# Kernel optimization log

Hardware: AMD Instinct MI355X
Metric: run time of the kernel (lower is better)

Reference implementation:

```python
import jax, jax.numpy as jnp
import numpy as np

B, N, D, CF = 8, 2048, 512, 128  # batch, nodes, feat_dim, count_feat


def setup_inputs() -> dict:
    key = jax.random.key(0)
    ks = jax.random.split(key, 12)
    s = 1.0 / np.sqrt(D)
    return {
        "X": jax.random.normal(ks[0], (B, N, D), jnp.float32),
        # first MultiHeadAttention (num_heads=1, mode='QK', out_features=feat_dim)
        "Wq1": jax.random.normal(ks[1], (D, D), jnp.float32) * s,
        "Wk1": jax.random.normal(ks[2], (D, D), jnp.float32) * s,
        "Wv1": jax.random.normal(ks[3], (D, D), jnp.float32) * s,
        "Wo1": jax.random.normal(ks[4], (D, D), jnp.float32) * s,
        # score attention (only its raw QK^T scores are used downstream)
        "Wq2": jax.random.normal(ks[5], (D, D), jnp.float32) * s,
        "Wk2": jax.random.normal(ks[6], (D, D), jnp.float32) * s,
        # count_mlp: Linear(D,CF) -> LeakyReLU(0.1) -> Linear(CF,1)
        "W1": jax.random.normal(ks[7], (D, CF), jnp.float32) * s,
        "b1": jnp.zeros((CF,), jnp.float32),
        "W2": jax.random.normal(ks[8], (CF, 1), jnp.float32) * (1.0 / np.sqrt(CF)),
        "b2": jnp.zeros((1,), jnp.float32),
    }


def reference(X, Wq1, Wk1, Wv1, Wo1, Wq2, Wk2, W1, b1, W2, b2):
    scale = 1.0 / jnp.sqrt(jnp.asarray(X.shape[-1], X.dtype))
    # --- first self-attention: att = softmax(QK^T/sqrt(d)) V Wo ---
    q1 = X @ Wq1
    k1 = X @ Wk1
    v1 = X @ Wv1
    s1 = jnp.einsum("bnd,bmd->bnm", q1, k1) * scale      # [B,N,N]
    p1 = jax.nn.softmax(s1, axis=-1)
    att = jnp.einsum("bnm,bmd->bnd", p1, v1) @ Wo1        # [B,N,D]
    # --- score attention over att: only raw scores are consumed ---
    s2 = jnp.einsum("bnd,bmd->bnm", att @ Wq2, att @ Wk2) * scale  # [B,N,N]
    # --- count_mlp threshold per node ---
    h = att @ W1 + b1
    h = jnp.where(h >= 0, h, 0.1 * h)                     # LeakyReLU(0.1)
    thresh = h @ W2 + b2                                  # [B,N,1]
    # --- mlp_score_thresh readout: clamp, row-normalize, clip ---
    surv = jnp.maximum(s2 - thresh, 0.0)                  # broadcast over last dim
    A = jnp.clip(surv / (jnp.sum(surv, axis=-1, keepdims=True) + 1e-9), 0.0, 1.0)
    return A
```

## Files before the change

kernel.cpp:

```cpp
#include <hip/hip_runtime.h>
#include <hip/hip_bf16.h>

#define BB 8
#define NN 2048
#define DD 512
#define CFF 128
#define MT (BB*NN)

typedef _Float16 half_t;
typedef __attribute__((ext_vector_type(8))) _Float16 half8;
typedef __attribute__((ext_vector_type(4))) float floatx4;
typedef __attribute__((ext_vector_type(4))) unsigned int uint4v;

#define MFMA16(a,b,c) __builtin_amdgcn_mfma_f32_16x16x32_f16((a),(b),(c),0,0,0)

template<int EPI>
__global__ __launch_bounds__(256) void gemm_f16s(
    const half_t* __restrict__ Ahi, const half_t* __restrict__ Alo, long lda, long sA,
    const half_t* __restrict__ Bhi, const half_t* __restrict__ Blo, long ldb, long sB,
    float* __restrict__ Cf, half_t* __restrict__ Chi, half_t* __restrict__ Clo, long ldc, long sC,
    int K, float alpha, const float* __restrict__ bias, const float* __restrict__ tvec)
{
    const int tid = threadIdx.x;
    const int row0 = blockIdx.y * 128, col0 = blockIdx.x * 128;
    const long z = blockIdx.z;
    const half_t* pAh = Ahi + z * sA + (long)row0 * lda;
    const half_t* pAl = Alo + z * sA + (long)row0 * lda;
    const half_t* pBh = Bhi + z * sB + (long)col0 * ldb;
    const half_t* pBl = Blo + z * sB + (long)col0 * ldb;

    __shared__ half_t lds[2][4][4096];

    const int l  = tid & 63;
    const int w  = tid >> 6;
    const int wr = w >> 1, wc = w & 1;
    const int Rw = wr * 64, Cw = wc * 64;
    const int rl = l & 15, kc = l >> 4;
    const int swz = (kc ^ (rl & 3)) * 8;

    floatx4 acc[4][4];
#pragma unroll
    for (int m = 0; m < 4; ++m)
#pragma unroll
        for (int n = 0; n < 4; ++n) acc[m][n] = (floatx4){0.f, 0.f, 0.f, 0.f};

    const int r0s = tid >> 2,         c0s = tid & 3;
    const int r1s = (tid + 256) >> 2, c1s = tid & 3;
    const int off0 = r0s * 32 + ((c0s ^ (r0s & 3)) * 8);
    const int off1 = r1s * 32 + ((c1s ^ (r1s & 3)) * 8);

    auto stage = [&](int buf, int k0) {
        long ga0 = (long)r0s * lda + k0 + c0s * 8;
        long gb0 = (long)r0s * ldb + k0 + c0s * 8;
        long ga1 = (long)r1s * lda + k0 + c1s * 8;
        long gb1 = (long)r1s * ldb + k0 + c1s * 8;
        uint4v a0 = *(const uint4v*)(pAh + ga0);
        uint4v a1 = *(const uint4v*)(pAl + ga0);
        uint4v b0 = *(const uint4v*)(pBh + gb0);
        uint4v b1 = *(const uint4v*)(pBl + gb0);
        uint4v a2 = *(const uint4v*)(pAh + ga1);
        uint4v a3 = *(const uint4v*)(pAl + ga1);
        uint4v b2 = *(const uint4v*)(pBh + gb1);
        uint4v b3 = *(const uint4v*)(pBl + gb1);
        *(uint4v*)&lds[buf][0][off0] = a0;
        *(uint4v*)&lds[buf][1][off0] = a1;
        *(uint4v*)&lds[buf][2][off0] = b0;
        *(uint4v*)&lds[buf][3][off0] = b1;
        *(uint4v*)&lds[buf][0][off1] = a2;
        *(uint4v*)&lds[buf][1][off1] = a3;
        *(uint4v*)&lds[buf][2][off1] = b2;
        *(uint4v*)&lds[buf][3][off1] = b3;
    };

    const int nk = K >> 5;
    stage(0, 0);
#pragma unroll 2
    for (int t = 0; t < nk; ++t) {
        __syncthreads();
        const int cur = t & 1;
        const half_t* bAh = &lds[cur][0][0];
        const half_t* bAl = &lds[cur][1][0];
        const half_t* bBh = &lds[cur][2][0];
        const half_t* bBl = &lds[cur][3][0];
        half8 af[4][2], bf[4][2];
#pragma unroll
        for (int m = 0; m < 4; ++m) {
            int off = (Rw + m * 16 + rl) * 32 + swz;
            af[m][0] = *(const half8*)(bAh + off);
            af[m][1] = *(const half8*)(bAl + off);
        }
#pragma unroll
        for (int n = 0; n < 4; ++n) {
            int off = (Cw + n * 16 + rl) * 32 + swz;
            bf[n][0] = *(const half8*)(bBh + off);
            bf[n][1] = *(const half8*)(bBl + off);
        }
#pragma unroll
        for (int m = 0; m < 4; ++m)
#pragma unroll
            for (int n = 0; n < 4; ++n) {
                acc[m][n] = MFMA16(af[m][0], bf[n][0], acc[m][n]);
                acc[m][n] = MFMA16(af[m][1], bf[n][0], acc[m][n]);
                acc[m][n] = MFMA16(af[m][0], bf[n][1], acc[m][n]);
            }
        if (t + 1 < nk) stage((t + 1) & 1, (t + 1) << 5);
    }

    const float* tv = (EPI == 3) ? (tvec + z * NN) : tvec;
#pragma unroll
    for (int m = 0; m < 4; ++m) {
#pragma unroll
        for (int n = 0; n < 4; ++n) {
            int col = col0 + Cw + n * 16 + rl;
#pragma unroll
            for (int r = 0; r < 4; ++r) {
                int row = row0 + Rw + m * 16 + kc * 4 + r;
                float v = acc[m][n][r];
                if (EPI == 0) {
                    Cf[z * sC + (long)row * ldc + col] = v * alpha;
                } else if (EPI == 1) {
                    half_t hh = (half_t)v;
                    long o = z * sC + (long)row * ldc + col;
                    Chi[o] = hh;
                    Clo[o] = (half_t)(v - (float)hh);
                } else if (EPI == 2) {
                    v += bias[col];
                    Cf[(long)row * ldc + col] = (v >= 0.f) ? v : 0.1f * v;
                } else {
                    Cf[z * sC + (long)row * ldc + col] = fmaxf(v * alpha - tv[row], 0.f);
                }
            }
        }
    }
}

__device__ __forceinline__ float waveReduceMax(float v) {
#pragma unroll
    for (int o = 32; o; o >>= 1) v = fmaxf(v, __shfl_down(v, o));
    return v;
}
__device__ __forceinline__ float waveReduceSum(float v) {
#pragma unroll
    for (int o = 32; o; o >>= 1) v += __shfl_down(v, o);
    return v;
}

__global__ __launch_bounds__(256) void softmax_split_kernel(float* __restrict__ S)
{
    __shared__ float red[4];
    __shared__ float fin;
    long row = blockIdx.x;
    float* p = S + row * (long)NN;
    half_t* ph = (half_t*)p;
    half_t* pl = ph + NN;
    int t = threadIdx.x;

    float4 v0 = *reinterpret_cast<float4*>(p + t * 8);
    float4 v1 = *reinterpret_cast<float4*>(p + t * 8 + 4);

    float m = fmaxf(fmaxf(fmaxf(v0.x, v0.y), fmaxf(v0.z, v0.w)),
                    fmaxf(fmaxf(v1.x, v1.y), fmaxf(v1.z, v1.w)));
    m = waveReduceMax(m);
    if ((t & 63) == 0) red[t >> 6] = m;
    __syncthreads();
    if (t == 0) fin = fmaxf(fmaxf(red[0], red[1]), fmaxf(red[2], red[3]));
    __syncthreads();
    m = fin;

    float e[8];
    e[0] = __expf(v0.x - m); e[1] = __expf(v0.y - m); e[2] = __expf(v0.z - m); e[3] = __expf(v0.w - m);
    e[4] = __expf(v1.x - m); e[5] = __expf(v1.y - m); e[6] = __expf(v1.z - m); e[7] = __expf(v1.w - m);
    float s = ((e[0] + e[1]) + (e[2] + e[3])) + ((e[4] + e[5]) + (e[6] + e[7]));
    s = waveReduceSum(s);
    __syncthreads();
    if ((t & 63) == 0) red[t >> 6] = s;
    __syncthreads();
    if (t == 0) fin = (red[0] + red[1]) + (red[2] + red[3]);
    __syncthreads();
    float inv = 1.0f / fin;

    __syncthreads();
    half8 hv, lv;
#pragma unroll
    for (int j = 0; j < 8; ++j) {
        float pv = e[j] * inv;
        half_t hh = (half_t)pv;
        hv[j] = hh;
        lv[j] = (half_t)(pv - (float)hh);
    }
    *(half8*)(ph + t * 8) = hv;
    *(half8*)(pl + t * 8) = lv;
}

__global__ __launch_bounds__(256) void rowsum_kernel(const float* __restrict__ S, float* __restrict__ sums)
{
    __shared__ float red[4];
    long row = blockIdx.x;
    const float* p = S + row * (long)NN;
    int t = threadIdx.x;
    float4 v0 = *reinterpret_cast<const float4*>(p + t * 8);
    float4 v1 = *reinterpret_cast<const float4*>(p + t * 8 + 4);
    float s = ((v0.x + v0.y) + (v0.z + v0.w)) + ((v1.x + v1.y) + (v1.z + v1.w));
    s = waveReduceSum(s);
    if ((t & 63) == 0) red[t >> 6] = s;
    __syncthreads();
    if (t == 0) sums[row] = (red[0] + red[1]) + (red[2] + red[3]);
}

__global__ __launch_bounds__(256) void norm_kernel(float* __restrict__ S, const float* __restrict__ sums)
{
    long i = (long)blockIdx.x * 256 + threadIdx.x;
    long base = i * 4;
    long row = base >> 11;
    float inv = 1.0f / (sums[row] + 1e-9f);
    float4 v = *reinterpret_cast<float4*>(S + base);
    v.x = fminf(v.x * inv, 1.0f);
    v.y = fminf(v.y * inv, 1.0f);
    v.z = fminf(v.z * inv, 1.0f);
    v.w = fminf(v.w * inv, 1.0f);
    *reinterpret_cast<float4*>(S + base) = v;
}

__global__ __launch_bounds__(64) void thresh_kernel(const float* __restrict__ h,
                                                    const float* __restrict__ W2,
                                                    const float* __restrict__ b2,
                                                    float* __restrict__ th)
{
    int row = blockIdx.x;
    int t = threadIdx.x;
    const float* hp = h + (long)row * CFF;
    float v = hp[t] * W2[t] + hp[t + 64] * W2[t + 64];
    v = waveReduceSum(v);
    if (t == 0) th[row] = v + b2[0];
}

__global__ __launch_bounds__(256) void wprep(const float* __restrict__ W,
                                             half_t* __restrict__ Th, half_t* __restrict__ Tl,
                                             int K, int N)
{
    __shared__ float tw[32][33];
    int n0 = blockIdx.x * 32, k0 = blockIdx.y * 32;
    int c = threadIdx.x & 31, r8 = threadIdx.x >> 5;
#pragma unroll
    for (int i = 0; i < 4; ++i) {
        int r = r8 + i * 8;
        tw[r][c] = W[(long)(k0 + r) * N + n0 + c];
    }
    __syncthreads();
#pragma unroll
    for (int i = 0; i < 4; ++i) {
        int nr = r8 + i * 8;
        float v = tw[c][nr];
        half_t hh = (half_t)v;
        Th[(long)(n0 + nr) * K + k0 + c] = hh;
        Tl[(long)(n0 + nr) * K + k0 + c] = (half_t)(v - (float)hh);
    }
}

__global__ __launch_bounds__(256) void split_f32(const float* __restrict__ in,
                                                 half_t* __restrict__ hi, half_t* __restrict__ lo)
{
    long i = ((long)blockIdx.x * 256 + threadIdx.x) * 8;
    float4 a = *(const float4*)(in + i), b = *(const float4*)(in + i + 4);
    float v[8] = {a.x, a.y, a.z, a.w, b.x, b.y, b.z, b.w};
    half8 hv, lv;
#pragma unroll
    for (int j = 0; j < 8; ++j) {
        half_t hh = (half_t)v[j];
        hv[j] = hh;
        lv[j] = (half_t)(v[j] - (float)hh);
    }
    *(half8*)(hi + i) = hv;
    *(half8*)(lo + i) = lv;
}

__global__ __launch_bounds__(256) void transpose_pair(const half_t* __restrict__ ih, const half_t* __restrict__ il,
                                                      half_t* __restrict__ oh, half_t* __restrict__ ol)
{
    __shared__ half_t th[64][66], tl[64][66];
    int b = blockIdx.z;
    int c0 = blockIdx.x * 64;
    int r0 = blockIdx.y * 64;
    const half_t* pih = ih + ((long)b * 2048 + r0) * 512 + c0;
    const half_t* pil = il + ((long)b * 2048 + r0) * 512 + c0;
    int t = threadIdx.x;
    int cc = (t & 7) * 8, rr = t >> 3;
#pragma unroll
    for (int i = 0; i < 2; ++i) {
        int r = rr + 32 * i;
        *(uint4v*)&th[r][cc] = *(const uint4v*)(pih + (long)r * 512 + cc);
        *(uint4v*)&tl[r][cc] = *(const uint4v*)(pil + (long)r * 512 + cc);
    }
    __syncthreads();
    half_t* poh = oh + ((long)b * 512 + c0) * 2048 + r0;
    half_t* pol = ol + ((long)b * 512 + c0) * 2048 + r0;
#pragma unroll
    for (int i = 0; i < 2; ++i) {
        int ic = rr + 32 * i;
        half8 vh, vl;
#pragma unroll
        for (int j = 0; j < 8; ++j) {
            vh[j] = th[cc + j][ic];
            vl[j] = tl[cc + j][ic];
        }
        *(half8*)(poh + (long)ic * 2048 + cc) = vh;
        *(half8*)(pol + (long)ic * 2048 + cc) = vl;
    }
}

static void launch_gemm16(hipStream_t s, int epi,
    const half_t* Ahi, const half_t* Alo, long lda, long sA,
    const half_t* Bhi, const half_t* Blo, long ldb, long sB,
    float* Cf, half_t* Chi, half_t* Clo, long ldc, long sC,
    int M, int N, int K, int batch, float alpha, const float* bias, const float* tvec)
{
    dim3 g(N / 128, M / 128, batch), b(256, 1, 1);
    if (epi == 0)      gemm_f16s<0><<<g, b, 0, s>>>(Ahi, Alo, lda, sA, Bhi, Blo, ldb, sB, Cf, Chi, Clo, ldc, sC, K, alpha, bias, tvec);
    else if (epi == 1) gemm_f16s<1><<<g, b, 0, s>>>(Ahi, Alo, lda, sA, Bhi, Blo, ldb, sB, Cf, Chi, Clo, ldc, sC, K, alpha, bias, tvec);
    else if (epi == 2) gemm_f16s<2><<<g, b, 0, s>>>(Ahi, Alo, lda, sA, Bhi, Blo, ldb, sB, Cf, Chi, Clo, ldc, sC, K, alpha, bias, tvec);
    else               gemm_f16s<3><<<g, b, 0, s>>>(Ahi, Alo, lda, sA, Bhi, Blo, ldb, sB, Cf, Chi, Clo, ldc, sC, K, alpha, bias, tvec);
}

extern "C" void kernel_launch(void* const* d_in, const int* in_sizes, int n_in,
                              void* d_out, int out_size, void* d_ws, size_t ws_size,
                              hipStream_t stream)
{
    const float* X   = (const float*)d_in[0];
    const float* Wq1 = (const float*)d_in[1];
    const float* Wk1 = (const float*)d_in[2];
    const float* Wv1 = (const float*)d_in[3];
    const float* Wo1 = (const float*)d_in[4];
    const float* Wq2 = (const float*)d_in[5];
    const float* Wk2 = (const float*)d_in[6];
    const float* W1  = (const float*)d_in[7];
    const float* b1  = (const float*)d_in[8];
    const float* W2  = (const float*)d_in[9];
    const float* b2  = (const float*)d_in[10];

    float* out = (float*)d_out;
    const float scale = 0.044194173824159216f;

    half_t* wsH = (half_t*)d_ws;
    const long U  = (long)MT * DD;
    const long WD = (long)DD * DD;
    half_t* sAh = wsH;          half_t* sAl = wsH + U;
    half_t* sBh = wsH + 2 * U;  half_t* sBl = wsH + 3 * U;
    half_t* sCh = wsH + 4 * U;  half_t* sCl = wsH + 5 * U;
    half_t* wt  = wsH + 6 * U;
    half_t* wq1h = wt;              half_t* wq1l = wq1h + WD;
    half_t* wk1h = wq1l + WD;       half_t* wk1l = wk1h + WD;
    half_t* wv1h = wk1l + WD;       half_t* wv1l = wv1h + WD;
    half_t* wo1h = wv1l + WD;       half_t* wo1l = wo1h + WD;
    half_t* wq2h = wo1l + WD;       half_t* wq2l = wq2h + WD;
    half_t* wk2h = wq2l + WD;       half_t* wk2l = wk2h + WD;
    half_t* w1h  = wk2l + WD;       half_t* w1l  = w1h + (long)DD * CFF;
    float*  thresh = (float*)(w1l + (long)DD * CFF);
    float*  sums   = thresh + MT;
    float* h = out;

    split_f32<<<dim3(4096), dim3(256), 0, stream>>>(X, sAh, sAl);
    wprep<<<dim3(16, 16), dim3(256), 0, stream>>>(Wq1, wq1h, wq1l, DD, DD);
    wprep<<<dim3(16, 16), dim3(256), 0, stream>>>(Wk1, wk1h, wk1l, DD, DD);
    wprep<<<dim3(16, 16), dim3(256), 0, stream>>>(Wv1, wv1h, wv1l, DD, DD);
    wprep<<<dim3(16, 16), dim3(256), 0, stream>>>(Wo1, wo1h, wo1l, DD, DD);
    wprep<<<dim3(16, 16), dim3(256), 0, stream>>>(Wq2, wq2h, wq2l, DD, DD);
    wprep<<<dim3(16, 16), dim3(256), 0, stream>>>(Wk2, wk2h, wk2l, DD, DD);
    wprep<<<dim3(4, 16),  dim3(256), 0, stream>>>(W1,  w1h,  w1l,  DD, CFF);

    launch_gemm16(stream, 1, sAh, sAl, DD, 0, wq1h, wq1l, DD, 0,
                  nullptr, sBh, sBl, DD, 0, MT, DD, DD, 1, 1.f, nullptr, nullptr);
    launch_gemm16(stream, 1, sAh, sAl, DD, 0, wk1h, wk1l, DD, 0,
                  nullptr, sCh, sCl, DD, 0, MT, DD, DD, 1, 1.f, nullptr, nullptr);

    launch_gemm16(stream, 0, sBh, sBl, DD, (long)NN * DD, sCh, sCl, DD, (long)NN * DD,
                  out, nullptr, nullptr, NN, (long)NN * NN, NN, NN, DD, BB, scale, nullptr, nullptr);

    launch_gemm16(stream, 1, sAh, sAl, DD, 0, wv1h, wv1l, DD, 0,
                  nullptr, sBh, sBl, DD, 0, MT, DD, DD, 1, 1.f, nullptr, nullptr);

    softmax_split_kernel<<<dim3(MT), dim3(256), 0, stream>>>(out);

    transpose_pair<<<dim3(8, 32, BB), dim3(256), 0, stream>>>(sBh, sBl, sCh, sCl);

    {
        const half_t* p1h = (const half_t*)d_out;
        const half_t* p1l = p1h + NN;
        launch_gemm16(stream, 1, p1h, p1l, 2 * NN, (long)NN * 2 * NN,
                      sCh, sCl, NN, (long)DD * NN,
                      nullptr, sBh, sBl, DD, (long)NN * DD, NN, DD, NN, BB, 1.f, nullptr, nullptr);
    }

    launch_gemm16(stream, 1, sBh, sBl, DD, 0, wo1h, wo1l, DD, 0,
                  nullptr, sCh, sCl, DD, 0, MT, DD, DD, 1, 1.f, nullptr, nullptr);

    launch_gemm16(stream, 1, sCh, sCl, DD, 0, wq2h, wq2l, DD, 0,
                  nullptr, sAh, sAl, DD, 0, MT, DD, DD, 1, 1.f, nullptr, nullptr);
    launch_gemm16(stream, 1, sCh, sCl, DD, 0, wk2h, wk2l, DD, 0,
                  nullptr, sBh, sBl, DD, 0, MT, DD, DD, 1, 1.f, nullptr, nullptr);

    launch_gemm16(stream, 2, sCh, sCl, DD, 0, w1h, w1l, DD, 0,
                  h, nullptr, nullptr, CFF, 0, MT, CFF, DD, 1, 1.f, b1, nullptr);

    thresh_kernel<<<dim3(MT), dim3(64), 0, stream>>>(h, W2, b2, thresh);

    launch_gemm16(stream, 3, sAh, sAl, DD, (long)NN * DD, sBh, sBl, DD, (long)NN * DD,
                  out, nullptr, nullptr, NN, (long)NN * NN, NN, NN, DD, BB, scale, nullptr, thresh);

    rowsum_kernel<<<dim3(MT), dim3(256), 0, stream>>>(out, sums);
    norm_kernel<<<dim3(out_size / 1024), dim3(256), 0, stream>>>(out, sums);
}
```

Before: 900.0 us.

## Fuse QK projections, thresh MLP and rowsum into GEMM epilogues; swizzle block order

Merges the Q/K projection GEMMs of both attentions into single wider GEMMs whose outputs are routed to separate slots, and folds the count-MLP second layer plus bias into the W1 GEMM epilogue through shuffle-reduced atomicAdds. The score GEMM epilogue now accumulates per-row sums with atomics, which removes the separate rowsum pass over the 128MB score matrix. It also adds a block-index remap across the grid and widens the norm kernel to 8 elements per thread. The atomics make the summation order nondeterministic and need a zero/bias initialisation kernel.

```diff
diff --git a/kernel.cpp b/kernel.cpp
--- a/kernel.cpp
+++ b/kernel.cpp
@@ -18,12 +18,23 @@
 __global__ __launch_bounds__(256) void gemm_f16s(
     const half_t* __restrict__ Ahi, const half_t* __restrict__ Alo, long lda, long sA,
     const half_t* __restrict__ Bhi, const half_t* __restrict__ Blo, long ldb, long sB,
-    float* __restrict__ Cf, half_t* __restrict__ Chi, half_t* __restrict__ Clo, long ldc, long sC,
-    int K, float alpha, const float* __restrict__ bias, const float* __restrict__ tvec)
-{
+    float* __restrict__ Cf, half_t* __restrict__ Chi, half_t* __restrict__ Clo,
+    long ldc, long sC, long slotS,
+    int K, float alpha, const float* __restrict__ bias, const float* __restrict__ tvec,
+    float* __restrict__ rsum)
+{
+    const int gx = gridDim.x, gy = gridDim.y;
+    int d = blockIdx.x + gx * (blockIdx.y + gy * blockIdx.z);
+    int total = gx * gy * gridDim.z;
+    int t0 = (d & 7) * (total >> 3) + (d >> 3);
+    int bx = t0 % gx;
+    int t1 = t0 / gx;
+    int by = t1 % gy;
+    int bz = t1 / gy;
+
     const int tid = threadIdx.x;
-    const int row0 = blockIdx.y * 128, col0 = blockIdx.x * 128;
-    const long z = blockIdx.z;
+    const int row0 = by * 128, col0 = bx * 128;
+    const long z = bz;
     const half_t* pAh = Ahi + z * sA + (long)row0 * lda;
     const half_t* pAl = Alo + z * sA + (long)row0 * lda;
     const half_t* pBh = Bhi + z * sB + (long)col0 * ldb;
@@ -106,29 +117,84 @@
         if (t + 1 < nk) stage((t + 1) & 1, (t + 1) << 5);
     }
 
-    const float* tv = (EPI == 3) ? (tvec + z * NN) : tvec;
-#pragma unroll
-    for (int m = 0; m < 4; ++m) {
-#pragma unroll
-        for (int n = 0; n < 4; ++n) {
-            int col = col0 + Cw + n * 16 + rl;
+    if (EPI == 0) {
+#pragma unroll
+        for (int m = 0; m < 4; ++m)
+#pragma unroll
+            for (int n = 0; n < 4; ++n) {
+                int col = col0 + Cw + n * 16 + rl;
+#pragma unroll
+                for (int r = 0; r < 4; ++r) {
+                    int row = row0 + Rw + m * 16 + kc * 4 + r;
+                    Cf[z * sC + (long)row * ldc + col] = acc[m][n][r] * alpha;
+                }
+            }
+    } else if (EPI == 1) {
+#pragma unroll
+        for (int m = 0; m < 4; ++m)
+#pragma unroll
+            for (int n = 0; n < 4; ++n) {
+                int col = col0 + Cw + n * 16 + rl;
+                long obase = (long)(col >> 9) * slotS + z * sC + (col & 511);
+#pragma unroll
+                for (int r = 0; r < 4; ++r) {
+                    int row = row0 + Rw + m * 16 + kc * 4 + r;
+                    long o = obase + (long)row * ldc;
+                    float v = acc[m][n][r];
+                    half_t hh = (half_t)v;
+                    Chi[o] = hh;
+                    Clo[o] = (half_t)(v - (float)hh);
+                }
+            }
+    } else if (EPI == 3) {
+        const float* tv = tvec + z * NN;
+        float* rs = rsum + z * NN;
+#pragma unroll
+        for (int m = 0; m < 4; ++m) {
 #pragma unroll
             for (int r = 0; r < 4; ++r) {
                 int row = row0 + Rw + m * 16 + kc * 4 + r;
-                float v = acc[m][n][r];
-                if (EPI == 0) {
-                    Cf[z * sC + (long)row * ldc + col] = v * alpha;
-                } else if (EPI == 1) {
-                    half_t hh = (half_t)v;
-                    long o = z * sC + (long)row * ldc + col;
-                    Chi[o] = hh;
-                    Clo[o] = (half_t)(v - (float)hh);
-                } else if (EPI == 2) {
-                    v += bias[col];
-                    Cf[(long)row * ldc + col] = (v >= 0.f) ? v : 0.1f * v;
-                } else {
-                    Cf[z * sC + (long)row * ldc + col] = fmaxf(v * alpha - tv[row], 0.f);
+                float tvr = tv[row];
+                float partial = 0.f;
+#pragma unroll
+                for (int n = 0; n < 4; ++n) {
+                    int col = col0 + Cw + n * 16 + rl;
+                    float v = fmaxf(acc[m][n][r] * alpha - tvr, 0.f);
+                    Cf[z * sC + (long)row * ldc + col] = v;
+                    partial += v;
                 }
+                partial += __shfl_xor(partial, 1);
+                partial += __shfl_xor(partial, 2);
+                partial += __shfl_xor(partial, 4);
+                partial += __shfl_xor(partial, 8);
+                if (rl == 0) atomicAdd(&rs[row], partial);
+            }
+        }
+    } else {
+        float w2v[4], bv[4];
+#pragma unroll
+        for (int n = 0; n < 4; ++n) {
+            int col = Cw + n * 16 + rl;
+            bv[n]  = bias[col];
+            w2v[n] = tvec[col];
+        }
+#pragma unroll
+        for (int m = 0; m < 4; ++m) {
+#pragma unroll
+            for (int r = 0; r < 4; ++r) {
+                int row = row0 + Rw + m * 16 + kc * 4 + r;
+                float partial = 0.f;
+#pragma unroll
+                for (int n = 0; n < 4; ++n) {
+                    float v = acc[m][n][r] + bv[n];
+                    v = (v >= 0.f) ? v : 0.1f * v;
+                    partial += v * w2v[n];
+                }
+                partial += __shfl_xor(partial, 1);
+                partial += __shfl_xor(partial, 2);
+                partial += __shfl_xor(partial, 4);
+                partial += __shfl_xor(partial, 8);
+                if (rl == 0) atomicAdd(&rsum[row], partial);
             }
         }
     }
@@ -192,46 +258,27 @@
     *(half8*)(pl + t * 8) = lv;
 }
 
-__global__ __launch_bounds__(256) void rowsum_kernel(const float* __restrict__ S, float* __restrict__ sums)
-{
-    __shared__ float red[4];
-    long row = blockIdx.x;
-    const float* p = S + row * (long)NN;
-    int t = threadIdx.x;
-    float4 v0 = *reinterpret_cast<const float4*>(p + t * 8);
-    float4 v1 = *reinterpret_cast<const float4*>(p + t * 8 + 4);
-    float s = ((v0.x + v0.y) + (v0.z + v0.w)) + ((v1.x + v1.y) + (v1.z + v1.w));
-    s = waveReduceSum(s);
-    if ((t & 63) == 0) red[t >> 6] = s;
-    __syncthreads();
-    if (t == 0) sums[row] = (red[0] + red[1]) + (red[2] + red[3]);
-}
-
 __global__ __launch_bounds__(256) void norm_kernel(float* __restrict__ S, const float* __restrict__ sums)
 {
     long i = (long)blockIdx.x * 256 + threadIdx.x;
-    long base = i * 4;
+    long base = i * 8;
     long row = base >> 11;
     float inv = 1.0f / (sums[row] + 1e-9f);
-    float4 v = *reinterpret_cast<float4*>(S + base);
-    v.x = fminf(v.x * inv, 1.0f);
-    v.y = fminf(v.y * inv, 1.0f);
-    v.z = fminf(v.z * inv, 1.0f);
-    v.w = fminf(v.w * inv, 1.0f);
-    *reinterpret_cast<float4*>(S + base) = v;
-}
-
-__global__ __launch_bounds__(64) void thresh_kernel(const float* __restrict__ h,
-                                                    const float* __restrict__ W2,
-                                                    const float* __restrict__ b2,
-                                                    float* __restrict__ th)
-{
-    int row = blockIdx.x;
-    int t = threadIdx.x;
-    const float* hp = h + (long)row * CFF;
-    float v = hp[t] * W2[t] + hp[t + 64] * W2[t + 64];
-    v = waveReduceSum(v);
-    if (t == 0) th[row] = v + b2[0];
+    float4 v0 = *reinterpret_cast<float4*>(S + base);
+    float4 v1 = *reinterpret_cast<float4*>(S + base + 4);
+    v0.x = fminf(v0.x * inv, 1.0f); v0.y = fminf(v0.y * inv, 1.0f);
+    v0.z = fminf(v0.z * inv, 1.0f); v0.w = fminf(v0.w * inv, 1.0f);
+    v1.x = fminf(v1.x * inv, 1.0f); v1.y = fminf(v1.y * inv, 1.0f);
+    v1.z = fminf(v1.z * inv, 1.0f); v1.w = fminf(v1.w * inv, 1.0f);
+    *reinterpret_cast<float4*>(S + base) = v0;
+    *reinterpret_cast<float4*>(S + base + 4) = v1;
+}
+
+__global__ __launch_bounds__(256) void init_aux(float* __restrict__ thresh, float* __restrict__ sums,
+                                                const float* __restrict__ b2)
+{
+    int i = blockIdx.x * 256 + threadIdx.x;
+    if (i < MT) { thresh[i] = b2[0]; sums[i] = 0.f; }
 }
 
 __global__ __launch_bounds__(256) void wprep(const float* __restrict__ W,
@@ -311,14 +358,15 @@
 static void launch_gemm16(hipStream_t s, int epi,
     const half_t* Ahi, const half_t* Alo, long lda, long sA,
     const half_t* Bhi, const half_t* Blo, long ldb, long sB,
-    float* Cf, half_t* Chi, half_t* Clo, long ldc, long sC,
-    int M, int N, int K, int batch, float alpha, const float* bias, const float* tvec)
+    float* Cf, half_t* Chi, half_t* Clo, long ldc, long sC, long slotS,
+    int M, int N, int K, int batch, float alpha,
+    const float* bias, const float* tvec, float* rsum)
 {
     dim3 g(N / 128, M / 128, batch), b(256, 1, 1);
-    if (epi == 0)      gemm_f16s<0><<<g, b, 0, s>>>(Ahi, Alo, lda, sA, Bhi, Blo, ldb, sB, Cf, Chi, Clo, ldc, sC, K, alpha, bias, tvec);
-    else if (epi == 1) gemm_f16s<1><<<g, b, 0, s>>>(Ahi, Alo, lda, sA, Bhi, Blo, ldb, sB, Cf, Chi, Clo, ldc, sC, K, alpha, bias, tvec);
-    else if (epi == 2) gemm_f16s<2><<<g, b, 0, s>>>(Ahi, Alo, lda, sA, Bhi, Blo, ldb, sB, Cf, Chi, Clo, ldc, sC, K, alpha, bias, tvec);
-    else               gemm_f16s<3><<<g, b, 0, s>>>(Ahi, Alo, lda, sA, Bhi, Blo, ldb, sB, Cf, Chi, Clo, ldc, sC, K, alpha, bias, tvec);
+    if (epi == 0)      gemm_f16s<0><<<g, b, 0, s>>>(Ahi, Alo, lda, sA, Bhi, Blo, ldb, sB, Cf, Chi, Clo, ldc, sC, slotS, K, alpha, bias, tvec, rsum);
+    else if (epi == 1) gemm_f16s<1><<<g, b, 0, s>>>(Ahi, Alo, lda, sA, Bhi, Blo, ldb, sB, Cf, Chi, Clo, ldc, sC, slotS, K, alpha, bias, tvec, rsum);
+    else if (epi == 3) gemm_f16s<3><<<g, b, 0, s>>>(Ahi, Alo, lda, sA, Bhi, Blo, ldb, sB, Cf, Chi, Clo, ldc, sC, slotS, K, alpha, bias, tvec, rsum);
+    else               gemm_f16s<4><<<g, b, 0, s>>>(Ahi, Alo, lda, sA, Bhi, Blo, ldb, sB, Cf, Chi, Clo, ldc, sC, slotS, K, alpha, bias, tvec, rsum);
 }
 
 extern "C" void kernel_launch(void* const* d_in, const int* in_sizes, int n_in,
@@ -347,36 +395,32 @@
     half_t* sBh = wsH + 2 * U;  half_t* sBl = wsH + 3 * U;
     half_t* sCh = wsH + 4 * U;  half_t* sCl = wsH + 5 * U;
     half_t* wt  = wsH + 6 * U;
-    half_t* wq1h = wt;              half_t* wq1l = wq1h + WD;
-    half_t* wk1h = wq1l + WD;       half_t* wk1l = wk1h + WD;
-    half_t* wv1h = wk1l + WD;       half_t* wv1l = wv1h + WD;
-    half_t* wo1h = wv1l + WD;       half_t* wo1l = wo1h + WD;
-    half_t* wq2h = wo1l + WD;       half_t* wq2l = wq2h + WD;
-    half_t* wk2h = wq2l + WD;       half_t* wk2l = wk2h + WD;
-    half_t* w1h  = wk2l + WD;       half_t* w1l  = w1h + (long)DD * CFF;
+    half_t* wqk1h = wt;               half_t* wqk1l = wqk1h + 2 * WD;
+    half_t* wv1h  = wqk1l + 2 * WD;   half_t* wv1l  = wv1h + WD;
+    half_t* wo1h  = wv1l + WD;        half_t* wo1l  = wo1h + WD;
+    half_t* wqk2h = wo1l + WD;        half_t* wqk2l = wqk2h + 2 * WD;
+    half_t* w1h   = wqk2l + 2 * WD;   half_t* w1l   = w1h + (long)DD * CFF;
     float*  thresh = (float*)(w1l + (long)DD * CFF);
     float*  sums   = thresh + MT;
-    float* h = out;
-
+
+    init_aux<<<dim3(64), dim3(256), 0, stream>>>(thresh, sums, b2);
     split_f32<<<dim3(4096), dim3(256), 0, stream>>>(X, sAh, sAl);
-    wprep<<<dim3(16, 16), dim3(256), 0, stream>>>(Wq1, wq1h, wq1l, DD, DD);
-    wprep<<<dim3(16, 16), dim3(256), 0, stream>>>(Wk1, wk1h, wk1l, DD, DD);
-    wprep<<<dim3(16, 16), dim3(256), 0, stream>>>(Wv1, wv1h, wv1l, DD, DD);
-    wprep<<<dim3(16, 16), dim3(256), 0, stream>>>(Wo1, wo1h, wo1l, DD, DD);
-    wprep<<<dim3(16, 16), dim3(256), 0, stream>>>(Wq2, wq2h, wq2l, DD, DD);
-    wprep<<<dim3(16, 16), dim3(256), 0, stream>>>(Wk2, wk2h, wk2l, DD, DD);
-    wprep<<<dim3(4, 16),  dim3(256), 0, stream>>>(W1,  w1h,  w1l,  DD, CFF);
-
-    launch_gemm16(stream, 1, sAh, sAl, DD, 0, wq1h, wq1l, DD, 0,
-                  nullptr, sBh, sBl, DD, 0, MT, DD, DD, 1, 1.f, nullptr, nullptr);
-    launch_gemm16(stream, 1, sAh, sAl, DD, 0, wk1h, wk1l, DD, 0,
-                  nullptr, sCh, sCl, DD, 0, MT, DD, DD, 1, 1.f, nullptr, nullptr);
+    wprep<<<dim3(16, 16), dim3(256), 0, stream>>>(Wq1, wqk1h,      wqk1l,      DD, DD);
+    wprep<<<dim3(16, 16), dim3(256), 0, stream>>>(Wk1, wqk1h + WD, wqk1l + WD, DD, DD);
+    wprep<<<dim3(16, 16), dim3(256), 0, stream>>>(Wv1, wv1h,  wv1l,  DD, DD);
+    wprep<<<dim3(16, 16), dim3(256), 0, stream>>>(Wo1, wo1h,  wo1l,  DD, DD);
+    wprep<<<dim3(16, 16), dim3(256), 0, stream>>>(Wq2, wqk2h,      wqk2l,      DD, DD);
+    wprep<<<dim3(16, 16), dim3(256), 0, stream>>>(Wk2, wqk2h + WD, wqk2l + WD, DD, DD);
+    wprep<<<dim3(4, 16),  dim3(256), 0, stream>>>(W1,  w1h,   w1l,   DD, CFF);
+
+    launch_gemm16(stream, 1, sAh, sAl, DD, 0, wqk1h, wqk1l, DD, 0,
+                  nullptr, sBh, sBl, DD, 0, 2 * U, MT, 2 * DD, DD, 1, 1.f, nullptr, nullptr, nullptr);
 
     launch_gemm16(stream, 0, sBh, sBl, DD, (long)NN * DD, sCh, sCl, DD, (long)NN * DD,
-                  out, nullptr, nullptr, NN, (long)NN * NN, NN, NN, DD, BB, scale, nullptr, nullptr);
+                  out, nullptr, nullptr, NN, (long)NN * NN, 0, NN, NN, DD, BB, scale, nullptr, nullptr, nullptr);
 
     launch_gemm16(stream, 1, sAh, sAl, DD, 0, wv1h, wv1l, DD, 0,
-                  nullptr, sBh, sBl, DD, 0, MT, DD, DD, 1, 1.f, nullptr, nullptr);
+                  nullptr, sBh, sBl, DD, 0, 0, MT, DD, DD, 1, 1.f, nullptr, nullptr, nullptr);
 
     softmax_split_kernel<<<dim3(MT), dim3(256), 0, stream>>>(out);
 
@@ -387,25 +431,20 @@
         const half_t* p1l = p1h + NN;
         launch_gemm16(stream, 1, p1h, p1l, 2 * NN, (long)NN * 2 * NN,
                       sCh, sCl, NN, (long)DD * NN,
-                      nullptr, sBh, sBl, DD, (long)NN * DD, NN, DD, NN, BB, 1.f, nullptr, nullptr);
+                      nullptr, sBh, sBl, DD, (long)NN * DD, 0, NN, DD, NN, BB, 1.f, nullptr, nullptr, nullptr);
     }
 
     launch_gemm16(stream, 1, sBh, sBl, DD, 0, wo1h, wo1l, DD, 0,
-                  nullptr, sCh, sCl, DD, 0, MT, DD, DD, 1, 1.f, nullptr, nullptr);
-
-    launch_gemm16(stream, 1, sCh, sCl, DD, 0, wq2h, wq2l, DD, 0,
-                  nullptr, sAh, sAl, DD, 0, MT, DD, DD, 1, 1.f, nullptr, nullptr);
-    launch_gemm16(stream, 1, sCh, sCl, DD, 0, wk2h, wk2l, DD, 0,
-                  nullptr, sBh, sBl, DD, 0, MT, DD, DD, 1, 1.f, nullptr, nullptr);
-
-    launch_gemm16(stream, 2, sCh, sCl, DD, 0, w1h, w1l, DD, 0,
-                  h, nullptr, nullptr, CFF, 0, MT, CFF, DD, 1, 1.f, b1, nullptr);
-
-    thresh_kernel<<<dim3(MT), dim3(64), 0, stream>>>(h, W2, b2, thresh);
+                  nullptr, sCh, sCl, DD, 0, 0, MT, DD, DD, 1, 1.f, nullptr, nullptr, nullptr);
+
+    launch_gemm16(stream, 1, sCh, sCl, DD, 0, wqk2h, wqk2l, DD, 0,
+                  nullptr, sAh, sAl, DD, 0, 2 * U, MT, 2 * DD, DD, 1, 1.f, nullptr, nullptr, nullptr);
+
+    launch_gemm16(stream, 4, sCh, sCl, DD, 0, w1h, w1l, DD, 0,
+                  nullptr, nullptr, nullptr, CFF, 0, 0, MT, CFF, DD, 1, 1.f, b1, W2, thresh);
 
     launch_gemm16(stream, 3, sAh, sAl, DD, (long)NN * DD, sBh, sBl, DD, (long)NN * DD,
-                  out, nullptr, nullptr, NN, (long)NN * NN, NN, NN, DD, BB, scale, nullptr, thresh);
-
-    rowsum_kernel<<<dim3(MT), dim3(256), 0, stream>>>(out, sums);
-    norm_kernel<<<dim3(out_size / 1024), dim3(256), 0, stream>>>(out, sums);
-}
+                  out, nullptr, nullptr, NN, (long)NN * NN, 0, NN, NN, DD, BB, scale, nullptr, thresh, sums);
+
+    norm_kernel<<<dim3(out_size / 2048), dim3(256), 0, stream>>>(out, sums);
+}
```

After: 808.3 us. -10.2%, faster.
